# Kernel optimization log

Hardware: AMD Instinct MI355X
Metric: run time of the kernel (lower is better)

## Reference

```python
import jax, jax.numpy as jnp
import numpy as np

EPS = 1e-5

def conv1x1(x, w, b):
    # x: [B,Cin,H,W], w: [Cout,Cin], b: [Cout]
    return jnp.einsum('oi,bihw->bohw', w, x) + b[None, :, None, None]

def self_attention(x, qw, qb, kw, kb, vw, vb, fw, fb):
    B, C, H, W = x.shape
    hid = qw.shape[0]
    q = conv1x1(x, qw, qb).reshape(B, hid, H * W).transpose(0, 2, 1)   # [B,HW,hid]
    k = conv1x1(x, kw, kb).reshape(B, hid, H * W)                      # [B,hid,HW]
    v = conv1x1(x, vw, vb).reshape(B, C, H * W)                        # [B,C,HW]
    attn = jax.nn.softmax(jnp.einsum('bnh,bhm->bnm', q, k), axis=-1)   # [B,HW,HW]
    z = jnp.einsum('bnm,bcm->bnc', attn, v)                            # [B,HW,C]
    # faithful to torch .view(B,C,H,W) on contiguous [B,HW,C]: raw reshape, no transpose
    z = z.reshape(B, C, H, W)
    return conv1x1(z * x, fw, fb) + x

def group_norm_per_channel(y, gw, gb):
    # GroupNorm(num_groups == num_channels): per-channel instance norm, biased var
    mean = y.mean(axis=(2, 3), keepdims=True)
    var = ((y - mean) ** 2).mean(axis=(2, 3), keepdims=True)
    yn = (y - mean) * jax.lax.rsqrt(var + EPS)
    return yn * gw[None, :, None, None] + gb[None, :, None, None]

def setup_inputs() -> dict:
    key = jax.random.key(0)
    ks = jax.random.split(key, 32)
    B, C, H, W = 4, 64, 64, 64
    hid, att = 64, 64
    d = {}
    d['x'] = jax.random.normal(ks[0], (B, C, H, W), jnp.float32)
    d['h'] = jax.random.normal(ks[1], (B, hid, H, W), jnp.float32)
    d['c'] = jax.random.normal(ks[2], (B, hid, H, W), jnp.float32)
    i = 3
    for pre, cin in (('ax', C), ('ah', hid)):
        for nm, cout in (('q', att), ('k', att), ('v', cin), ('f', cin)):
            d[f'{pre}_{nm}w'] = jax.random.normal(ks[i], (cout, cin), jnp.float32) * 0.05; i += 1
            d[f'{pre}_{nm}b'] = jax.random.normal(ks[i], (cout,), jnp.float32) * 0.05; i += 1
    d['conv_w'] = jax.random.normal(ks[i], (4 * hid, C + hid, 3, 3), jnp.float32) * 0.05; i += 1
    d['conv_b'] = jax.random.normal(ks[i], (4 * hid,), jnp.float32) * 0.05; i += 1
    d['gn_w'] = jnp.ones((4 * hid,), jnp.float32)
    d['gn_b'] = jnp.zeros((4 * hid,), jnp.float32)
    return d

def reference(x, h, c,
              ax_qw, ax_qb, ax_kw, ax_kb, ax_vw, ax_vb, ax_fw, ax_fb,
              ah_qw, ah_qb, ah_kw, ah_kb, ah_vw, ah_vb, ah_fw, ah_fb,
              conv_w, conv_b, gn_w, gn_b):
    hid = h.shape[1]
    xa = self_attention(x, ax_qw, ax_qb, ax_kw, ax_kb, ax_vw, ax_vb, ax_fw, ax_fb)
    ha = self_attention(h, ah_qw, ah_qb, ah_kw, ah_kb, ah_vw, ah_vb, ah_fw, ah_fb)
    combined = jnp.concatenate([xa, ha], axis=1)
    y = jax.lax.conv_general_dilated(
        combined, conv_w, window_strides=(1, 1), padding=[(1, 1), (1, 1)],
        dimension_numbers=('NCHW', 'OIHW', 'NCHW')) + conv_b[None, :, None, None]
    y = group_norm_per_channel(y, gn_w, gn_b)
    i, f, o, g = jnp.split(y, 4, axis=1)
    i = jax.nn.sigmoid(i); f = jax.nn.sigmoid(f); o = jax.nn.sigmoid(o); g = jnp.tanh(g)
    c_next = f * c + i * g
    h_next = o * jnp.tanh(c_next)
    return jnp.stack([h_next, c_next])  # [2,B,hid,H,W]
```

## Files before the change

### kernel.cpp

```cpp
#include <hip/hip_runtime.h>
#include <hip/hip_bf16.h>


typedef __hip_bfloat16 bf16;
typedef const __hip_bfloat16* bfp;
typedef short bf16x8 __attribute__((ext_vector_type(8)));
typedef short short4v __attribute__((ext_vector_type(4)));
typedef float f32x4 __attribute__((ext_vector_type(4)));

#define SM_SHIFT 12.0f

__device__ __forceinline__ float ldf(const void* p, long i, int f32) {
    return f32 ? ((const float*)p)[i]
               : __bfloat162float(((const bf16*)p)[i]);
}
__device__ __forceinline__ short f2bf(float f) {
    bf16 h = __float2bfloat16(f);
    return *reinterpret_cast<short*>(&h);
}

__device__ __forceinline__ int sniff_f32(const void* xr)
{
    int lane = threadIdx.x & 63;
    unsigned long long v = ((const unsigned long long*)xr)[lane];
    int ok = 0;
#pragma unroll
    for (int i = 0; i < 4; ++i) {
        int e = (int)((v >> (16 * i + 7)) & 0xFF);
        ok += (e >= 100 && e <= 141);
    }
    ok += __shfl_xor(ok, 1, 64);
    ok += __shfl_xor(ok, 2, 64);
    ok += __shfl_xor(ok, 4, 64);
    ok += __shfl_xor(ok, 8, 64);
    ok += __shfl_xor(ok, 16, 64);
    ok += __shfl_xor(ok, 32, 64);
    return ok < 200;
}

__global__ __launch_bounds__(256) void qkv_kernel(
    const void* __restrict__ Xx, const void* __restrict__ Xh,
    const void* __restrict__ qwx, const void* __restrict__ qbx,
    const void* __restrict__ kwx, const void* __restrict__ kbx,
    const void* __restrict__ vwx, const void* __restrict__ vbx,
    const void* __restrict__ qwh, const void* __restrict__ qbh,
    const void* __restrict__ kwh, const void* __restrict__ kbh,
    const void* __restrict__ vwh, const void* __restrict__ vbh,
    bf16* __restrict__ Qx, bf16* __restrict__ Kx, bf16* __restrict__ Vtx,
    bf16* __restrict__ Qh, bf16* __restrict__ Kh, bf16* __restrict__ Vth,
    const void* __restrict__ cw, bf16* __restrict__ Wt,
    float* __restrict__ gacc, int qkvN)
{
    int bx = blockIdx.x;
    int tid = threadIdx.x;
    int f32 = sniff_f32(Xx);
    if (bx >= qkvN) {
        if (bx == qkvN) {
            for (int j = 0; j < 8; ++j)
                gacc[tid * 8 + j] = 0.f;
        }
        int wi = (bx - qkvN) * 256 + tid;
        int tap = wi >> 15;
        int rem = wi & 32767;
        int oc = rem >> 7, ic = rem & 127;
        Wt[wi] = __float2bfloat16(ldf(cw, ((long)oc * 128 + ic) * 9 + tap, f32));
        return;
    }
    __shared__ __align__(16) short xt[64][72];
    __shared__ __align__(16) short wq[64][72];
    __shared__ __align__(16) short wk[64][72];
    __shared__ __align__(16) short wv[64][72];
    int ab  = (bx >> 8) & 1;
    int idx = bx & 255;
    int b = idx >> 6;
    int n0 = (idx & 63) * 64;
    int wave = tid >> 6, lane = tid & 63;
    int q = lane >> 4, l15 = lane & 15;

    const void* X = ab ? Xh : Xx;
    const void* qw = ab ? qwh : qwx; const void* qb = ab ? qbh : qbx;
    const void* kw = ab ? kwh : kwx; const void* kb = ab ? kbh : kbx;
    const void* vw = ab ? vwh : vwx; const void* vb = ab ? vbh : vbx;
    short* Qg  = (short*)(ab ? Qh  : Qx)  + (long)b * 262144;
    short* Kg  = (short*)(ab ? Kh  : Kx)  + (long)b * 262144;
    short* Vtg = (short*)(ab ? Vth : Vtx) + (long)b * 262144;

    if (!f32) {
        const short* q16 = (const short*)qw;
        const short* k16 = (const short*)kw;
        const short* v16 = (const short*)vw;
        for (int rep = 0; rep < 2; ++rep) {
            int j8 = (rep * 256 + tid) * 8;
            *(bf16x8*)&wq[j8 >> 6][j8 & 63] = *(const bf16x8*)(q16 + j8);
            *(bf16x8*)&wk[j8 >> 6][j8 & 63] = *(const bf16x8*)(k16 + j8);
            *(bf16x8*)&wv[j8 >> 6][j8 & 63] = *(const bf16x8*)(v16 + j8);
        }
    } else {
        for (int rep = 0; rep < 16; ++rep) {
            int j = rep * 256 + tid;
            int i = j >> 6, cc = j & 63;
            wq[i][cc] = f2bf(((const float*)qw)[j]);
            wk[i][cc] = f2bf(((const float*)kw)[j]);
            wv[i][cc] = f2bf(((const float*)vw)[j]);
        }
    }
    long xbase = (long)b * 262144;
    for (int rep = 0; rep < 16; ++rep) {
        int c = rep * 4 + (tid >> 6);
        int p = tid & 63;
        xt[p][c] = f2bf(ldf(X, xbase + (long)c * 4096 + n0 + p, f32));
    }
    __syncthreads();

    bf16x8 a0 = *(const bf16x8*)&xt[wave * 16 + l15][q * 8];
    bf16x8 a1 = *(const bf16x8*)&xt[wave * 16 + l15][32 + q * 8];

    for (int ct = 0; ct < 4; ++ct) {
        bf16x8 bq0 = *(const bf16x8*)&wq[ct * 16 + l15][q * 8];
        bf16x8 bq1 = *(const bf16x8*)&wq[ct * 16 + l15][32 + q * 8];
        f32x4 z = (f32x4){0.f, 0.f, 0.f, 0.f};
        z = __builtin_amdgcn_mfma_f32_16x16x32_bf16(a0, bq0, z, 0, 0, 0);
        z = __builtin_amdgcn_mfma_f32_16x16x32_bf16(a1, bq1, z, 0, 0, 0);
        float bias = ldf(qb, ct * 16 + l15, f32);
        for (int reg = 0; reg < 4; ++reg)
            Qg[(long)(n0 + wave * 16 + q * 4 + reg) * 64 + ct * 16 + l15] =
                f2bf(z[reg] + bias);
    }
    for (int ct = 0; ct < 4; ++ct) {
        bf16x8 bk0 = *(const bf16x8*)&wk[ct * 16 + l15][q * 8];
        bf16x8 bk1 = *(const bf16x8*)&wk[ct * 16 + l15][32 + q * 8];
        f32x4 z = (f32x4){0.f, 0.f, 0.f, 0.f};
        z = __builtin_amdgcn_mfma_f32_16x16x32_bf16(a0, bk0, z, 0, 0, 0);
        z = __builtin_amdgcn_mfma_f32_16x16x32_bf16(a1, bk1, z, 0, 0, 0);
        float bias = ldf(kb, ct * 16 + l15, f32);
        for (int reg = 0; reg < 4; ++reg)
            Kg[(long)(n0 + wave * 16 + q * 4 + reg) * 64 + ct * 16 + l15] =
                f2bf(z[reg] + bias);
    }
    bf16x8 av0 = *(const bf16x8*)&wv[wave * 16 + l15][q * 8];
    bf16x8 av1 = *(const bf16x8*)&wv[wave * 16 + l15][32 + q * 8];
    for (int ct = 0; ct < 4; ++ct) {
        bf16x8 bx0 = *(const bf16x8*)&xt[ct * 16 + l15][q * 8];
        bf16x8 bx1 = *(const bf16x8*)&xt[ct * 16 + l15][32 + q * 8];
        f32x4 z = (f32x4){0.f, 0.f, 0.f, 0.f};
        z = __builtin_amdgcn_mfma_f32_16x16x32_bf16(av0, bx0, z, 0, 0, 0);
        z = __builtin_amdgcn_mfma_f32_16x16x32_bf16(av1, bx1, z, 0, 0, 0);
        for (int reg = 0; reg < 4; ++reg) {
            int c_out = wave * 16 + q * 4 + reg;
            float bias = ldf(vb, c_out, f32);
            Vtg[(long)c_out * 4096 + n0 + ct * 16 + l15] = f2bf(z[reg] + bias);
        }
    }
}

__global__ __launch_bounds__(256, 2) void attn_kernel(
    bfp Qx, bfp Kx, bfp Vtx, bf16* Ox,
    bfp Qh, bfp Kh, bfp Vth, bf16* Oh,
    float* __restrict__ lw, int split)
{
    __shared__ __align__(16) short ks [2][64][64];
    __shared__ __align__(16) short vts[2][64][64];
    __shared__ __align__(16) short ps[4][16][64];
    int tid = threadIdx.x;
    int wave = tid >> 6, lane = tid & 63;
    int q = lane >> 4, l15 = lane & 15;
    int idx = blockIdx.x & 255;
    int ab, half, mstart, ntile;
    if (split) {
        ab = blockIdx.x >> 9; half = (blockIdx.x >> 8) & 1;
        mstart = half * 2048; ntile = 32;
    } else {
        ab = blockIdx.x >> 8; half = 0; mstart = 0; ntile = 64;
    }
    int b = idx >> 6;
    int rt = idx & 63;
    int n0 = rt * 64 + wave * 16;
    const short* Qb  = (const short*)(ab ? Qh  : Qx)  + (long)b * 262144;
    const short* Kb  = (const short*)(ab ? Kh  : Kx)  + (long)b * 262144;
    const short* Vtb = (const short*)(ab ? Vth : Vtx) + (long)b * 262144;
    short* Ob = (short*)(ab ? Oh : Ox) + (long)half * (1l << 20) + (long)b * 262144;

    bf16x8 aq0 = *(const bf16x8*)(Qb + (long)(n0 + l15) * 64 + q * 8);
    bf16x8 aq1 = *(const bf16x8*)(Qb + (long)(n0 + l15) * 64 + 32 + q * 8);

    f32x4 acc_o[4];
    for (int ct = 0; ct < 4; ++ct) acc_o[ct] = (f32x4){0.f, 0.f, 0.f, 0.f};
    float l_part[4] = {0.f, 0.f, 0.f, 0.f};

    int swp = (l15 >> 1) & 7;
    int c0 = (q ^ swp) << 3;
    int c1 = ((q + 4) ^ swp) << 3;
    int sw_s = (tid >> 4) & 7;
    int cs = (((tid & 7) ^ sw_s)) << 3;

    int r0 = tid >> 3, r1 = r0 + 32;
    bf16x8 pk0 = *(const bf16x8*)(Kb + (long)(mstart + r0) * 64 + (tid & 7) * 8);
    bf16x8 pk1 = *(const bf16x8*)(Kb + (long)(mstart + r1) * 64 + (tid & 7) * 8);
    bf16x8 pv0 = *(const bf16x8*)(Vtb + (long)r0 * 4096 + mstart + (tid & 7) * 8);
    bf16x8 pv1 = *(const bf16x8*)(Vtb + (long)r1 * 4096 + mstart + (tid & 7) * 8);

    for (int it = 0; it < ntile; ++it) {
        int buf = it & 1;
        *(bf16x8*)&ks[buf][r0][cs]  = pk0;
        *(bf16x8*)&ks[buf][r1][cs]  = pk1;
        *(bf16x8*)&vts[buf][r0][cs] = pv0;
        *(bf16x8*)&vts[buf][r1][cs] = pv1;
        __syncthreads();
        if (it + 1 < ntile) {
            long m = (long)mstart + (long)(it + 1) * 64;
            pk0 = *(const bf16x8*)(Kb + (m + r0) * 64 + (tid & 7) * 8);
            pk1 = *(const bf16x8*)(Kb + (m + r1) * 64 + (tid & 7) * 8);
            pv0 = *(const bf16x8*)(Vtb + (long)r0 * 4096 + m + (tid & 7) * 8);
            pv1 = *(const bf16x8*)(Vtb + (long)r1 * 4096 + m + (tid & 7) * 8);
        }

        f32x4 s[4];
        for (int t = 0; t < 4; ++t) {
            const short* krow = &ks[buf][t * 16 + l15][0];
            bf16x8 bk0 = *(const bf16x8*)(krow + c0);
            bf16x8 bk1 = *(const bf16x8*)(krow + c1);
            f32x4 z = (f32x4){0.f, 0.f, 0.f, 0.f};
            z    = __builtin_amdgcn_mfma_f32_16x16x32_bf16(aq0, bk0, z, 0, 0, 0);
            s[t] = __builtin_amdgcn_mfma_f32_16x16x32_bf16(aq1, bk1, z, 0, 0, 0);
        }

        for (int t = 0; t < 4; ++t) {
            int chunkbase = t << 1 | (l15 >> 3);
            for (int reg = 0; reg < 4; ++reg) {
                float p = __expf(fminf(s[t][reg] - SM_SHIFT, 60.f));
                l_part[reg] += p;
                int n = q * 4 + reg;
                int swn = (n >> 1) & 7;
                ps[wave][n][((chunkbase ^ swn) << 3) | (l15 & 7)] = f2bf(p);
            }
        }

        const short* prow = &ps[wave][l15][0];
        bf16x8 bp0 = *(const bf16x8*)(prow + c0);
        bf16x8 bp1 = *(const bf16x8*)(prow + c1);
        for (int ct = 0; ct < 4; ++ct) {
            const short* vrow = &vts[buf][ct * 16 + l15][0];
            bf16x8 av0 = *(const bf16x8*)(vrow + c0);
            bf16x8 av1 = *(const bf16x8*)(vrow + c1);
            acc_o[ct] = __builtin_amdgcn_mfma_f32_16x16x32_bf16(av0, bp0, acc_o[ct], 0, 0, 0);
            acc_o[ct] = __builtin_amdgcn_mfma_f32_16x16x32_bf16(av1, bp1, acc_o[ct], 0, 0, 0);
        }
    }

    for (int reg = 0; reg < 4; ++reg) {
        l_part[reg] += __shfl_xor(l_part[reg], 1, 64);
        l_part[reg] += __shfl_xor(l_part[reg], 2, 64);
        l_part[reg] += __shfl_xor(l_part[reg], 4, 64);
        l_part[reg] += __shfl_xor(l_part[reg], 8, 64);
    }
    if (split) {
        if (l15 == 0) {
            float* lp = lw + (long)ab * 32768 + (long)half * 16384
                           + (long)b * 4096 + n0 + q * 4;
            lp[0] = l_part[0]; lp[1] = l_part[1];
            lp[2] = l_part[2]; lp[3] = l_part[3];
        }
        for (int ct = 0; ct < 4; ++ct) {
            short* dst = Ob + (long)(n0 + l15) * 64 + ct * 16 + q * 4;
            dst[0] = f2bf(acc_o[ct][0]);
            dst[1] = f2bf(acc_o[ct][1]);
            dst[2] = f2bf(acc_o[ct][2]);
            dst[3] = f2bf(acc_o[ct][3]);
        }
    } else {
        int src = (l15 >> 2) << 4;
        float L0 = __shfl(l_part[0], src, 64);
        float L1 = __shfl(l_part[1], src, 64);
        float L2 = __shfl(l_part[2], src, 64);
        float L3 = __shfl(l_part[3], src, 64);
        int r3 = l15 & 3;
        float ln = (r3 == 0) ? L0 : (r3 == 1) ? L1 : (r3 == 2) ? L2 : L3;
        float iln = 1.f / ln;
        for (int ct = 0; ct < 4; ++ct) {
            short* dst = Ob + (long)(n0 + l15) * 64 + ct * 16 + q * 4;
            dst[0] = f2bf(acc_o[ct][0] * iln);
            dst[1] = f2bf(acc_o[ct][1] * iln);
            dst[2] = f2bf(acc_o[ct][2] * iln);
            dst[3] = f2bf(acc_o[ct][3] * iln);
        }
    }
}

__global__ __launch_bounds__(256) void attnout_kernel(
    bfp Ox, const void* __restrict__ Xx,
    const void* __restrict__ fwx, const void* __restrict__ fbx,
    bf16* __restrict__ outx,
    bfp Oh, const void* __restrict__ Xh,
    const void* __restrict__ fwh, const void* __restrict__ fbh,
    bf16* __restrict__ outh,
    const float* __restrict__ lw, int split)
{
    __shared__ __align__(16) short fwt[64][72];
    __shared__ __align__(16) short at [64][72];
    int f32 = sniff_f32(Xx);
    int ab  = blockIdx.x >> 8;
    int idx = blockIdx.x & 255;
    int b = idx >> 6;
    int h = idx & 63;
    int tid = threadIdx.x;
    int wave = tid >> 6, lane = tid & 63;
    int q = lane >> 4, l15 = lane & 15;
    bfp O = ab ? Oh : Ox;
    const void* X = ab ? Xh : Xx;
    const void* fw = ab ? fwh : fwx;
    const void* fb = ab ? fbh : fbx;
    bf16* out = ab ? outh : outx;

    if (!f32) {
        const short* f16p = (const short*)fw;
        for (int rep = 0; rep < 2; ++rep) {
            int j8 = (rep * 256 + tid) * 8;
            *(bf16x8*)&fwt[j8 >> 6][j8 & 63] = *(const bf16x8*)(f16p + j8);
        }
    } else {
        for (int rep = 0; rep < 16; ++rep) {
            int j = rep * 256 + tid;
            fwt[j >> 6][j & 63] = f2bf(((const float*)fw)[j]);
        }
    }
    const bf16* Ob0 = O + (long)b * 262144;
    const bf16* Ob1 = Ob0 + (1l << 20);
    const float* lp0 = lw + (long)ab * 32768 + (long)b * 4096;
    const float* lp1 = lp0 + 16384;
    long xbase = (long)b * 262144;
    {
        int w = tid & 63;
        for (int rep = 0; rep < 16; ++rep) {
            int cn = rep * 4 + (tid >> 6);
            int n = cn * 64 + h;
            float o;
            if (split) {
                float iln = 1.f / (lp0[n] + lp1[n]);
                o = (__bfloat162float(Ob0[(long)n * 64 + w]) +
                     __bfloat162float(Ob1[(long)n * 64 + w])) * iln;
            } else {
                o = __bfloat162float(Ob0[(long)n * 64 + w]);
            }
            float prod = o * ldf(X, xbase + (long)cn * 4096 + h * 64 + w, f32);
            at[w][cn] = f2bf(prod);
        }
    }
    __syncthreads();
    bf16x8 a0 = *(const bf16x8*)&fwt[wave * 16 + l15][q * 8];
    bf16x8 a1 = *(const bf16x8*)&fwt[wave * 16 + l15][32 + q * 8];
    short* outp = (short*)out;
    for (int nt = 0; nt < 4; ++nt) {
        bf16x8 b0 = *(const bf16x8*)&at[nt * 16 + l15][q * 8];
        bf16x8 b1 = *(const bf16x8*)&at[nt * 16 + l15][32 + q * 8];
        f32x4 z = (f32x4){0.f, 0.f, 0.f, 0.f};
        z = __builtin_amdgcn_mfma_f32_16x16x32_bf16(a0, b0, z, 0, 0, 0);
        z = __builtin_amdgcn_mfma_f32_16x16x32_bf16(a1, b1, z, 0, 0, 0);
        int w = nt * 16 + l15;
        short4v o4;
        for (int reg = 0; reg < 4; ++reg) {
            int o = wave * 16 + q * 4 + reg;
            float v = z[reg] + ldf(fb, o, f32) +
                      ldf(X, xbase + (long)o * 4096 + h * 64 + w, f32);
            o4[reg] = f2bf(v);
        }
        *(short4v*)(outp + (((long)(b * 64 + h) * 64 + w) * 64 + wave * 16 + q * 4)) = o4;
    }
}

__global__ __launch_bounds__(256) void conv3x3_kernel(
    bfp xa, bfp ha, bfp Wt, const void* __restrict__ cb,
    bf16* __restrict__ y, float* __restrict__ gacc,
    const void* __restrict__ xraw)
{
    __shared__ __align__(16) short in_s[3][66][136];
    int f32 = sniff_f32(xraw);
    int bx = blockIdx.x;
    int b = bx >> 7;
    int rem = bx & 127;
    int h = rem >> 1;
    int halfoc = rem & 1;
    int tid = threadIdx.x;
    int wave = tid >> 6, lane = tid & 63;
    int q = lane >> 4, l15 = lane & 15;

    const short* xab = (const short*)xa + (long)b * 262144;
    const short* hab = (const short*)ha + (long)b * 262144;
    const bf16x8 zv = {0, 0, 0, 0, 0, 0, 0, 0};
    for (int r = 0; r < 3; ++r) {
        int gy = h + r - 1;
        bool valid = (gy >= 0) && (gy < 64);
        for (int s = 0; s < 2; ++s) {
            int strip = s * 256 + tid;
            int w = strip >> 3;
            int c8 = (strip & 7) * 8;
            bf16x8 vx = zv, vh = zv;
            if (valid) {
                vx = *(const bf16x8*)(xab + ((long)gy * 64 + w) * 64 + c8);
                vh = *(const bf16x8*)(hab + ((long)gy * 64 + w) * 64 + c8);
            }
            *(bf16x8*)&in_s[r][w + 1][c8]      = vx;
            *(bf16x8*)&in_s[r][w + 1][64 + c8] = vh;
        }
    }
    if (tid < 96) {
        int r = tid / 32;
        int rest = tid % 32;
        int col = (rest & 1) ? 65 : 0;
        int c8 = (rest >> 1) * 8;
        *(bf16x8*)&in_s[r][col][c8] = zv;
    }
    __syncthreads();

    int oc0 = halfoc * 128 + wave * 32;
    f32x4 acc[2][4];
    for (int mt = 0; mt < 2; ++mt)
        for (int nt = 0; nt < 4; ++nt)
            acc[mt][nt] = (f32x4){0.f, 0.f, 0.f, 0.f};

    const short* Wb = (const short*)Wt;
    for (int tap = 0; tap < 9; ++tap) {
        int dy = tap / 3, dx = tap - dy * 3;
        for (int kc = 0; kc < 4; ++kc) {
            bf16x8 afrag[2];
            for (int mt = 0; mt < 2; ++mt)
                afrag[mt] = *(const bf16x8*)(
                    Wb + ((long)tap * 256 + oc0 + mt * 16 + l15) * 128 + kc * 32 + q * 8);
            for (int nt = 0; nt < 4; ++nt) {
                bf16x8 bfrag = *(const bf16x8*)&in_s[dy][nt * 16 + l15 + dx][kc * 32 + q * 8];
                for (int mt = 0; mt < 2; ++mt)
                    acc[mt][nt] = __builtin_amdgcn_mfma_f32_16x16x32_bf16(
                        afrag[mt], bfrag, acc[mt][nt], 0, 0, 0);
            }
        }
    }

    long ybase = (long)b * 1048576 + (long)h * 64;
    for (int mt = 0; mt < 2; ++mt) {
        for (int reg = 0; reg < 4; ++reg) {
            int oc = oc0 + mt * 16 + q * 4 + reg;
            float bias = ldf(cb, oc, f32);
            float s = 0.f, s2 = 0.f;
            for (int nt = 0; nt < 4; ++nt) {
                float v = acc[mt][nt][reg] + bias;
                ((short*)y)[ybase + (long)oc * 4096 + nt * 16 + l15] = f2bf(v);
                s += v; s2 = fmaf(v, v, s2);
            }
            s  += __shfl_xor(s,  1, 64);  s2 += __shfl_xor(s2, 1, 64);
            s  += __shfl_xor(s,  2, 64);  s2 += __shfl_xor(s2, 2, 64);
            s  += __shfl_xor(s,  4, 64);  s2 += __shfl_xor(s2, 4, 64);
            s  += __shfl_xor(s,  8, 64);  s2 += __shfl_xor(s2, 8, 64);
            if (l15 == 0) {
                atomicAdd(&gacc[b * 256 + oc], s);
                atomicAdd(&gacc[1024 + b * 256 + oc], s2);
            }
        }
    }
}

__global__ __launch_bounds__(256) void gates_kernel(
    bfp y, const float* __restrict__ gacc,
    const void* __restrict__ gw, const void* __restrict__ gb,
    const void* __restrict__ c_in, void* __restrict__ out)
{
    int f32 = sniff_f32(c_in);
    int idx = blockIdx.x * 256 + threadIdx.x;
    int b = idx >> 18;
    int r = idx & 262143;
    int ch = r >> 12;
    int pix = r & 4095;
    long ybase = (long)b * 1048576;
    float vals[4];
    for (int g = 0; g < 4; ++g) {
        int cc = g * 64 + ch;
        float mu  = gacc[b * 256 + cc] * (1.f / 4096.f);
        float var = gacc[1024 + b * 256 + cc] * (1.f / 4096.f) - mu * mu;
        float rstd = rsqrtf(fmaxf(var, 0.f) + 1e-5f);
        float v = __bfloat162float(y[ybase + (long)cc * 4096 + pix]);
        v = (v - mu) * rstd * ldf(gw, cc, f32) + ldf(gb, cc, f32);
        vals[g] = v;
    }
    float ig = 1.f / (1.f + __expf(-vals[0]));
    float fg = 1.f / (1.f + __expf(-vals[1]));
    float og = 1.f / (1.f + __expf(-vals[2]));
    float gg = tanhf(vals[3]);
    float cprev = ldf(c_in, idx, f32);
    float cn = fg * cprev + ig * gg;
    float hn = og * tanhf(cn);
    if (f32) {
        float* o32 = (float*)out;
        o32[idx] = hn;
        o32[1048576 + idx] = cn;
    } else {
        bf16* o16 = (bf16*)out;
        o16[idx] = __float2bfloat16(hn);
        o16[1048576 + idx] = __float2bfloat16(cn);
    }
}

extern "C" void kernel_launch(void* const* d_in, const int* in_sizes, int n_in,
                              void* d_out, int out_size, void* d_ws, size_t ws_size,
                              hipStream_t stream)
{
    const void* x = d_in[0]; const void* h = d_in[1]; const void* c = d_in[2];
    const void* ax_qw = d_in[3],  *ax_qb = d_in[4];
    const void* ax_kw = d_in[5],  *ax_kb = d_in[6];
    const void* ax_vw = d_in[7],  *ax_vb = d_in[8];
    const void* ax_fw = d_in[9],  *ax_fb = d_in[10];
    const void* ah_qw = d_in[11], *ah_qb = d_in[12];
    const void* ah_kw = d_in[13], *ah_kb = d_in[14];
    const void* ah_vw = d_in[15], *ah_vb = d_in[16];
    const void* ah_fw = d_in[17], *ah_fb = d_in[18];
    const void* conv_w = d_in[19], *conv_b = d_in[20];
    const void* gn_w = d_in[21],  *gn_b = d_in[22];

    char* wsb = (char*)d_ws;
    auto S = [&](int i) { return wsb + ((unsigned long)i << 21); };
    bool splitm = ws_size >= (27ul << 20);
    bool fused  = splitm || ws_size >= (18ul << 20) + 16384;

    bf16* ha = (bf16*)S(0);
    bf16* Wt = (bf16*)S(1);
    bf16 *Qx, *Kx, *Vtx, *Qh, *Kh, *Vth, *xa, *y, *Ox, *Oh;
    char* tail;
    if (splitm) {
        Qx = (bf16*)S(2); Kx = (bf16*)S(3); Vtx = (bf16*)S(4);
        Qh = (bf16*)S(5); Kh = (bf16*)S(6); Vth = (bf16*)S(7);
        xa = (bf16*)S(8);
        Ox = (bf16*)S(9);
        Oh = (bf16*)S(11);
        y = Qx;
        tail = S(13);
    } else if (fused) {
        Qx = (bf16*)S(2); Kx = (bf16*)S(3); Vtx = (bf16*)S(4);
        Qh = (bf16*)S(5); Kh = (bf16*)S(6); Vth = (bf16*)S(7);
        xa = (bf16*)S(8); Ox = Qx; Oh = Qh; y = Qx;
        tail = S(9);
    } else {
        Qx = (bf16*)S(2); Kx = (bf16*)S(3); Vtx = (bf16*)S(4);
        Qh = Qx; Kh = Kx; Vth = Vtx;
        xa = (bf16*)S(6); Ox = Qx; Oh = Qh; y = Qx;
        tail = S(7);
    }
    float* gacc = (float*)tail;
    float* lw   = (float*)(tail + 8192);

    if (fused) {
        qkv_kernel<<<512 + 1152, 256, 0, stream>>>(
            x, h,
            ax_qw, ax_qb, ax_kw, ax_kb, ax_vw, ax_vb,
            ah_qw, ah_qb, ah_kw, ah_kb, ah_vw, ah_vb,
            Qx, Kx, Vtx, Qh, Kh, Vth, conv_w, Wt, gacc, 512);
        if (splitm) {
            attn_kernel<<<1024, 256, 0, stream>>>(
                Qx, Kx, Vtx, Ox, Qh, Kh, Vth, Oh, lw, 1);
            attnout_kernel<<<512, 256, 0, stream>>>(
                Ox, x, ax_fw, ax_fb, xa, Oh, h, ah_fw, ah_fb, ha, lw, 1);
        } else {
            attn_kernel<<<512, 256, 0, stream>>>(
                Qx, Kx, Vtx, Ox, Qh, Kh, Vth, Oh, lw, 0);
            attnout_kernel<<<512, 256, 0, stream>>>(
                Ox, x, ax_fw, ax_fb, xa, Oh, h, ah_fw, ah_fb, ha, lw, 0);
        }
    } else {
        qkv_kernel<<<256 + 1152, 256, 0, stream>>>(
            x, x,
            ax_qw, ax_qb, ax_kw, ax_kb, ax_vw, ax_vb,
            ax_qw, ax_qb, ax_kw, ax_kb, ax_vw, ax_vb,
            Qx, Kx, Vtx, Qx, Kx, Vtx, conv_w, Wt, gacc, 256);
        attn_kernel<<<256, 256, 0, stream>>>(
            Qx, Kx, Vtx, Ox, Qx, Kx, Vtx, Ox, lw, 0);
        attnout_kernel<<<256, 256, 0, stream>>>(
            Ox, x, ax_fw, ax_fb, xa, Ox, x, ax_fw, ax_fb, xa, lw, 0);
        qkv_kernel<<<256, 256, 0, stream>>>(
            h, h,
            ah_qw, ah_qb, ah_kw, ah_kb, ah_vw, ah_vb,
            ah_qw, ah_qb, ah_kw, ah_kb, ah_vw, ah_vb,
            Qh, Kh, Vth, Qh, Kh, Vth, conv_w, Wt, gacc, 256);
        attn_kernel<<<256, 256, 0, stream>>>(
            Qh, Kh, Vth, Oh, Qh, Kh, Vth, Oh, lw, 0);
        attnout_kernel<<<256, 256, 0, stream>>>(
            Oh, h, ah_fw, ah_fb, ha, Oh, h, ah_fw, ah_fb, ha, lw, 0);
    }
    conv3x3_kernel<<<512, 256, 0, stream>>>(xa, ha, Wt, conv_b, y, gacc, x);
    gates_kernel<<<4096, 256, 0, stream>>>(y, gacc, gn_w, gn_b, c, d_out);
}
```

Baseline: 236.2 us.

## Compute S transposed and shuffle P in registers instead of through LDS

Swaps the MFMA operand order so the score tile comes out transposed (keys along registers, queries along lanes). The softmax probabilities are packed to bf16 pairs and rearranged with cross-lane xor shuffles straight into the B-operand layout for the PV MFMA. This removes the per-wave LDS scratch buffer and its scattered 2-byte stores and reloads. The row-sum reduction also collapses to two shuffles. The cost is eight extra cross-lane shuffles per tile and a more intricate lane-mapping that must exactly match the MFMA operand layout.

```diff
diff --git a/kernel.cpp b/kernel.cpp
--- a/kernel.cpp
+++ b/kernel.cpp
@@ -7,6 +7,7 @@
 typedef short bf16x8 __attribute__((ext_vector_type(8)));
 typedef short short4v __attribute__((ext_vector_type(4)));
 typedef float f32x4 __attribute__((ext_vector_type(4)));
+typedef unsigned int u32x4 __attribute__((ext_vector_type(4)));
 
 #define SM_SHIFT 12.0f
 
@@ -17,6 +18,12 @@
 __device__ __forceinline__ short f2bf(float f) {
     bf16 h = __float2bfloat16(f);
     return *reinterpret_cast<short*>(&h);
+}
+__device__ __forceinline__ void xbswap(unsigned& a, unsigned& b, int mask, bool up) {
+    unsigned s = up ? a : b;
+    unsigned r = __shfl_xor(s, mask, 64);
+    a = up ? r : a;
+    b = up ? b : r;
 }
 
 __device__ __forceinline__ int sniff_f32(const void* xr)
@@ -160,7 +167,6 @@
 {
     __shared__ __align__(16) short ks [2][64][64];
     __shared__ __align__(16) short vts[2][64][64];
-    __shared__ __align__(16) short ps[4][16][64];
     int tid = threadIdx.x;
     int wave = tid >> 6, lane = tid & 63;
     int q = lane >> 4, l15 = lane & 15;
@@ -185,13 +191,16 @@
 
     f32x4 acc_o[4];
     for (int ct = 0; ct < 4; ++ct) acc_o[ct] = (f32x4){0.f, 0.f, 0.f, 0.f};
-    float l_part[4] = {0.f, 0.f, 0.f, 0.f};
+    float l_acc = 0.f;
 
     int swp = (l15 >> 1) & 7;
     int c0 = (q ^ swp) << 3;
     int c1 = ((q + 4) ^ swp) << 3;
     int sw_s = (tid >> 4) & 7;
     int cs = (((tid & 7) ^ sw_s)) << 3;
+
+    bool up5 = (lane & 32) != 0;
+    bool up4 = (lane & 16) != 0;
 
     int r0 = tid >> 3, r1 = r0 + 32;
     bf16x8 pk0 = *(const bf16x8*)(Kb + (long)(mstart + r0) * 64 + (tid & 7) * 8);
@@ -215,29 +224,45 @@
         }
 
         f32x4 s[4];
+#pragma unroll
         for (int t = 0; t < 4; ++t) {
             const short* krow = &ks[buf][t * 16 + l15][0];
-            bf16x8 bk0 = *(const bf16x8*)(krow + c0);
-            bf16x8 bk1 = *(const bf16x8*)(krow + c1);
+            bf16x8 ak0 = *(const bf16x8*)(krow + c0);
+            bf16x8 ak1 = *(const bf16x8*)(krow + c1);
             f32x4 z = (f32x4){0.f, 0.f, 0.f, 0.f};
-            z    = __builtin_amdgcn_mfma_f32_16x16x32_bf16(aq0, bk0, z, 0, 0, 0);
-            s[t] = __builtin_amdgcn_mfma_f32_16x16x32_bf16(aq1, bk1, z, 0, 0, 0);
-        }
-
+            z    = __builtin_amdgcn_mfma_f32_16x16x32_bf16(ak0, aq0, z, 0, 0, 0);
+            s[t] = __builtin_amdgcn_mfma_f32_16x16x32_bf16(ak1, aq1, z, 0, 0, 0);
+        }
+
+        unsigned P32[8];
+        float lt = 0.f;
+#pragma unroll
         for (int t = 0; t < 4; ++t) {
-            int chunkbase = t << 1 | (l15 >> 3);
-            for (int reg = 0; reg < 4; ++reg) {
-                float p = __expf(fminf(s[t][reg] - SM_SHIFT, 60.f));
-                l_part[reg] += p;
-                int n = q * 4 + reg;
-                int swn = (n >> 1) & 7;
-                ps[wave][n][((chunkbase ^ swn) << 3) | (l15 & 7)] = f2bf(p);
-            }
-        }
-
-        const short* prow = &ps[wave][l15][0];
-        bf16x8 bp0 = *(const bf16x8*)(prow + c0);
-        bf16x8 bp1 = *(const bf16x8*)(prow + c1);
+            float p0 = __expf(fminf(s[t][0] - SM_SHIFT, 60.f));
+            float p1 = __expf(fminf(s[t][1] - SM_SHIFT, 60.f));
+            float p2 = __expf(fminf(s[t][2] - SM_SHIFT, 60.f));
+            float p3 = __expf(fminf(s[t][3] - SM_SHIFT, 60.f));
+            lt += (p0 + p1) + (p2 + p3);
+            P32[t * 2] = (unsigned)(unsigned short)f2bf(p0)
+                       | ((unsigned)(unsigned short)f2bf(p1) << 16);
+            P32[t * 2 + 1] = (unsigned)(unsigned short)f2bf(p2)
+                           | ((unsigned)(unsigned short)f2bf(p3) << 16);
+        }
+        l_acc += lt;
+
+        xbswap(P32[0], P32[2], 32, up5);
+        xbswap(P32[1], P32[3], 32, up5);
+        xbswap(P32[4], P32[6], 32, up5);
+        xbswap(P32[5], P32[7], 32, up5);
+        xbswap(P32[0], P32[2], 16, up4);
+        xbswap(P32[1], P32[3], 16, up4);
+        xbswap(P32[4], P32[6], 16, up4);
+        xbswap(P32[5], P32[7], 16, up4);
+        u32x4 B0v = (u32x4){P32[0], P32[1], P32[2], P32[3]};
+        u32x4 B1v = (u32x4){P32[4], P32[5], P32[6], P32[7]};
+        bf16x8 bp0 = __builtin_bit_cast(bf16x8, B0v);
+        bf16x8 bp1 = __builtin_bit_cast(bf16x8, B1v);
+
         for (int ct = 0; ct < 4; ++ct) {
             const short* vrow = &vts[buf][ct * 16 + l15][0];
             bf16x8 av0 = *(const bf16x8*)(vrow + c0);
@@ -247,18 +272,13 @@
         }
     }
 
-    for (int reg = 0; reg < 4; ++reg) {
-        l_part[reg] += __shfl_xor(l_part[reg], 1, 64);
-        l_part[reg] += __shfl_xor(l_part[reg], 2, 64);
-        l_part[reg] += __shfl_xor(l_part[reg], 4, 64);
-        l_part[reg] += __shfl_xor(l_part[reg], 8, 64);
-    }
+    l_acc += __shfl_xor(l_acc, 16, 64);
+    l_acc += __shfl_xor(l_acc, 32, 64);
+
     if (split) {
-        if (l15 == 0) {
-            float* lp = lw + (long)ab * 32768 + (long)half * 16384
-                           + (long)b * 4096 + n0 + q * 4;
-            lp[0] = l_part[0]; lp[1] = l_part[1];
-            lp[2] = l_part[2]; lp[3] = l_part[3];
+        if (lane < 16) {
+            lw[(long)ab * 32768 + (long)half * 16384
+               + (long)b * 4096 + n0 + lane] = l_acc;
         }
         for (int ct = 0; ct < 4; ++ct) {
             short* dst = Ob + (long)(n0 + l15) * 64 + ct * 16 + q * 4;
@@ -268,14 +288,7 @@
             dst[3] = f2bf(acc_o[ct][3]);
         }
     } else {
-        int src = (l15 >> 2) << 4;
-        float L0 = __shfl(l_part[0], src, 64);
-        float L1 = __shfl(l_part[1], src, 64);
-        float L2 = __shfl(l_part[2], src, 64);
-        float L3 = __shfl(l_part[3], src, 64);
-        int r3 = l15 & 3;
-        float ln = (r3 == 0) ? L0 : (r3 == 1) ? L1 : (r3 == 2) ? L2 : L3;
-        float iln = 1.f / ln;
+        float iln = 1.f / l_acc;
         for (int ct = 0; ct < 4; ++ct) {
             short* dst = Ob + (long)(n0 + l15) * 64 + ct * 16 + q * 4;
             dst[0] = f2bf(acc_o[ct][0] * iln);
```

Measured after the change: 232.6 us. About the same (-1.5%).
